# Kernel tuning notes

Hardware: AMD Instinct MI355X
Metric: run time of the kernel (lower is better)

Reference implementation:

```python
import jax, jax.numpy as jnp
import numpy as np

N_HEADS = 16


def setup_inputs() -> dict:
    key = jax.random.key(0)
    ks = jax.random.split(key, 12)
    B, S, D = 2, 2048, 1024
    inp = {
        "query": jax.random.normal(ks[0], (B, S, D), jnp.float32),
        "key": jax.random.normal(ks[1], (B, S, D), jnp.float32),
        "value": jax.random.normal(ks[2], (B, S, D), jnp.float32),
        "mask": jnp.ones((B, S), jnp.int32),
        "Wq": jax.random.normal(ks[3], (D, D), jnp.float32) * 0.02,
        "bq": jax.random.normal(ks[4], (D,), jnp.float32) * 0.02,
        "Wk": jax.random.normal(ks[5], (D, D), jnp.float32) * 0.02,
        "bk": jax.random.normal(ks[6], (D,), jnp.float32) * 0.02,
        "Wv": jax.random.normal(ks[7], (D, D), jnp.float32) * 0.02,
        "bv": jax.random.normal(ks[8], (D,), jnp.float32) * 0.02,
        "Wo": jax.random.normal(ks[9], (D, D), jnp.float32) * 0.02,
        "bo": jax.random.normal(ks[10], (D,), jnp.float32) * 0.02,
    }
    return inp


def _shape(x, bs, n_heads, d_head):
    # (bs, seq, dim) -> (bs, n_heads, seq, d_head)
    return x.reshape(bs, -1, n_heads, d_head).transpose(0, 2, 1, 3)


def reference(query, key, value, mask, Wq, bq, Wk, bk, Wv, bv, Wo, bo):
    bs, q_len, dim = query.shape
    d_head = dim // N_HEADS

    q = _shape(query @ Wq + bq, bs, N_HEADS, d_head) / jnp.sqrt(jnp.asarray(d_head, query.dtype))
    k = _shape(key @ Wk + bk, bs, N_HEADS, d_head)
    v = _shape(value @ Wv + bv, bs, N_HEADS, d_head)

    scores = jnp.einsum("bhqd,bhkd->bhqk", q, k)  # [bs, h, q_len, k_len]
    neg = jnp.finfo(scores.dtype).min
    scores = jnp.where((mask == 0)[:, None, None, :], neg, scores)
    weights = jax.nn.softmax(scores, axis=-1)  # dropout p=0 -> identity

    context = jnp.einsum("bhqk,bhkd->bhqd", weights, v)
    context = context.transpose(0, 2, 1, 3).reshape(bs, q_len, dim)
    return context @ Wo + bo
```

## Files before the change

### kernel.cpp

```cpp
#include <hip/hip_runtime.h>
#include <hip/hip_bf16.h>
#include <stdint.h>

typedef short s16x8 __attribute__((ext_vector_type(8)));
typedef float f32x4 __attribute__((ext_vector_type(4)));
typedef float f32x16 __attribute__((ext_vector_type(16)));

union FragU { uint4 u; s16x8 v; };

static __device__ __forceinline__ uint32_t pk2bf(float a, float b) {
  union { __hip_bfloat162 h; uint32_t u; } cv;
  cv.h = __float22bfloat162_rn(make_float2(a, b));
  return cv.u;
}

static __device__ __forceinline__ unsigned short f2bf(float f) {
  union { float f; uint32_t u; } x; x.f = f;
  uint32_t r = x.u + 0x7FFFu + ((x.u >> 16) & 1u);
  return (unsigned short)(r >> 16);
}

static __device__ __forceinline__ void gl_lds16(const void* g, void* lds_wave_base) {
  __builtin_amdgcn_global_load_lds(
      (const __attribute__((address_space(1))) uint32_t*)(uintptr_t)g,
      (__attribute__((address_space(3))) uint32_t*)(uintptr_t)lds_wave_base, 16, 0, 0);
}

__global__ __launch_bounds__(256) void wt4_kernel(const float* __restrict__ W0,
                                                  const float* __restrict__ W1,
                                                  const float* __restrict__ W2,
                                                  const float* __restrict__ W3,
                                                  unsigned short* __restrict__ T0,
                                                  unsigned short* __restrict__ T1,
                                                  unsigned short* __restrict__ T2,
                                                  unsigned short* __restrict__ T3) {
  __shared__ unsigned short tile[64][68];
  const int z = blockIdx.z;
  const float* W = (z == 0) ? W0 : (z == 1) ? W1 : (z == 2) ? W2 : W3;
  unsigned short* WT = (z == 0) ? T0 : (z == 1) ? T1 : (z == 2) ? T2 : T3;
  const int t = threadIdx.x;
  const int n0 = blockIdx.x * 64, k0 = blockIdx.y * 64;
  const int r = t >> 4, c4 = (t & 15) * 4;
#pragma unroll
  for (int i = 0; i < 4; ++i) {
    const int k = i * 16 + r;
    const float4 v = *(const float4*)&W[(k0 + k) * 1024 + n0 + c4];
    tile[k][c4 + 0] = f2bf(v.x);
    tile[k][c4 + 1] = f2bf(v.y);
    tile[k][c4 + 2] = f2bf(v.z);
    tile[k][c4 + 3] = f2bf(v.w);
  }
  __syncthreads();
#pragma unroll
  for (int i = 0; i < 4; ++i) {
    const int n = i * 16 + r;
    ushort4 o;
    o.x = tile[c4 + 0][n];
    o.y = tile[c4 + 1][n];
    o.z = tile[c4 + 2][n];
    o.w = tile[c4 + 3][n];
    *(ushort4*)&WT[(n0 + n) * 1024 + k0 + c4] = o;
  }
}

__global__ __launch_bounds__(256, 2) void qkv_gemm(const float* __restrict__ Aq,
                                                   const float* __restrict__ Ak,
                                                   const float* __restrict__ Av,
                                                   const unsigned short* __restrict__ Wq,
                                                   const unsigned short* __restrict__ Wk,
                                                   const unsigned short* __restrict__ Wv,
                                                   const float* __restrict__ bq,
                                                   const float* __restrict__ bk,
                                                   const float* __restrict__ bv,
                                                   unsigned short* __restrict__ Qb,
                                                   unsigned short* __restrict__ Kb,
                                                   unsigned short* __restrict__ Vt,
                                                   const float qscale) {
  __shared__ char AsB[3][128 * 128];
  __shared__ char BsB[3][128 * 64];
  const int t = threadIdx.x;
  const int z = blockIdx.z;
  const float* A = (z == 0) ? Aq : (z == 1) ? Ak : Av;
  const unsigned short* BT = (z == 0) ? Wq : (z == 1) ? Wk : Wv;
  const float* bias = (z == 0) ? bq : (z == 1) ? bk : bv;
  const float scale = (z == 0) ? qscale : 1.0f;

  const int lane = t & 63, w = t >> 6;
  const int g = lane >> 4, li = lane & 15;
  const int wr = (w >> 1) * 64, wc = (w & 1) * 64;
  const int lin = blockIdx.x + 8 * blockIdx.y;
  const int work = (lin & 7) * 32 + (lin >> 3);
  const int m0 = (work >> 3) * 128, n0 = (work & 7) * 128;

  const int br1 = t >> 2, bg1 = (t & 3) ^ ((br1 >> 1) & 3);
  const int br2 = br1 + 64, bg2 = (t & 3) ^ ((br2 >> 1) & 3);
  int arow[4], acol[4];
#pragma unroll
  for (int i = 0; i < 4; ++i) {
    const int c = t + 256 * i;
    const int row = c >> 3, sl = (c >> 1) & 3, hf = c & 1;
    arow[i] = row;
    acol[i] = ((sl ^ (row & 3)) << 3) + ((hf ^ ((row >> 2) & 1)) << 2);
  }

  auto stage = [&](int kt, int buf) {
    const int k0 = kt * 32;
    char* bb = &BsB[buf][0] + (w << 10);
    gl_lds16(BT + (size_t)(n0 + br1) * 1024 + k0 + bg1 * 8, bb);
    gl_lds16(BT + (size_t)(n0 + br2) * 1024 + k0 + bg2 * 8, bb + 4096);
#pragma unroll
    for (int i = 0; i < 4; ++i)
      gl_lds16(A + (size_t)(m0 + arow[i]) * 1024 + k0 + acol[i],
               &AsB[buf][0] + i * 4096 + (w << 10));
  };

  f32x4 acc[4][4] = {};
  stage(0, 0);
  stage(1, 1);
  asm volatile("s_waitcnt vmcnt(6)" ::: "memory");
  asm volatile("s_barrier" ::: "memory");

  int cur = 0;
  for (int kt = 0; kt < 32; ++kt) {
    if (kt < 30) {
      int nb = cur + 2; if (nb >= 3) nb -= 3;
      stage(kt + 2, nb);
    }
    const char* Ab = &AsB[cur][0];
    const char* Bb = &BsB[cur][0];
    FragU a[4], bf[4];
#pragma unroll
    for (int i = 0; i < 4; ++i) {
      const int ra = wr + i * 16 + li;
      const int hsw = ((ra >> 2) & 1) << 4;
      const char* pa = Ab + ra * 128 + ((g ^ (ra & 3)) << 5);
      const float4 fa0 = *(const float4*)(pa + hsw);
      const float4 fa1 = *(const float4*)(pa + (16 ^ hsw));
      a[i].u = uint4{pk2bf(fa0.x, fa0.y), pk2bf(fa0.z, fa0.w),
                     pk2bf(fa1.x, fa1.y), pk2bf(fa1.z, fa1.w)};
      const int rb = wc + i * 16 + li;
      bf[i].u = *(const uint4*)(Bb + rb * 64 + ((g ^ ((rb >> 1) & 3)) << 4));
    }
#pragma unroll
    for (int fm = 0; fm < 4; ++fm)
#pragma unroll
      for (int fn = 0; fn < 4; ++fn)
        acc[fm][fn] = __builtin_amdgcn_mfma_f32_16x16x32_bf16(a[fm].v, bf[fn].v, acc[fm][fn], 0, 0, 0);

    if (kt < 30) {
      asm volatile("s_waitcnt vmcnt(6)" ::: "memory");
    } else if (kt == 30) {
      asm volatile("s_waitcnt vmcnt(0)" ::: "memory");
    }
    if (kt < 31) asm volatile("s_barrier" ::: "memory");
    cur = (cur == 2) ? 0 : cur + 1;
  }

  unsigned short* OutN = (z == 0) ? Qb : Kb;
#pragma unroll
  for (int fn = 0; fn < 4; ++fn) {
    const int n = n0 + wc + fn * 16 + li;
    const float bv2 = bias[n];
#pragma unroll
    for (int fm = 0; fm < 4; ++fm) {
      const int mb = m0 + wr + fm * 16 + g * 4;
      const f32x4 v = acc[fm][fn];
      ushort4 pk;
      pk.x = f2bf((v[0] + bv2) * scale);
      pk.y = f2bf((v[1] + bv2) * scale);
      pk.z = f2bf((v[2] + bv2) * scale);
      pk.w = f2bf((v[3] + bv2) * scale);
      if (z == 2) {
        const int bb = mb >> 11, s = mb & 2047;
        *(ushort4*)&Vt[(size_t)(bb * 1024 + n) * 2048 + s] = pk;
      } else {
        unsigned short* o = OutN;
        o[(size_t)(mb + 0) * 1024 + n] = pk.x;
        o[(size_t)(mb + 1) * 1024 + n] = pk.y;
        o[(size_t)(mb + 2) * 1024 + n] = pk.z;
        o[(size_t)(mb + 3) * 1024 + n] = pk.w;
      }
    }
  }
}

__global__ __launch_bounds__(256, 2) void out_gemm(const unsigned short* __restrict__ A,
                                                   const unsigned short* __restrict__ BT,
                                                   const float* __restrict__ bias,
                                                   float* __restrict__ Out) {
  __shared__ char AsB[3][128 * 64];
  __shared__ char BsB[3][128 * 64];
  const int t = threadIdx.x;
  const int lane = t & 63, w = t >> 6;
  const int g = lane >> 4, li = lane & 15;
  const int wr = (w >> 1) * 64, wc = (w & 1) * 64;
  const int lin = blockIdx.x + 8 * blockIdx.y;
  const int work = (lin & 7) * 32 + (lin >> 3);
  const int m0 = (work >> 3) * 128, n0 = (work & 7) * 128;

  const int r1 = t >> 2, g1 = (t & 3) ^ ((r1 >> 1) & 3);
  const int r2 = r1 + 64, g2 = (t & 3) ^ ((r2 >> 1) & 3);

  auto stage = [&](int kt, int buf) {
    const int k0 = kt * 32;
    gl_lds16(BT + (size_t)(n0 + r1) * 1024 + k0 + g1 * 8, &BsB[buf][0] + (w << 10));
    gl_lds16(BT + (size_t)(n0 + r2) * 1024 + k0 + g2 * 8, &BsB[buf][0] + 4096 + (w << 10));
    gl_lds16(A + (size_t)(m0 + r1) * 1024 + k0 + g1 * 8, &AsB[buf][0] + (w << 10));
    gl_lds16(A + (size_t)(m0 + r2) * 1024 + k0 + g2 * 8, &AsB[buf][0] + 4096 + (w << 10));
  };

  f32x4 acc[4][4] = {};
  stage(0, 0);
  stage(1, 1);
  asm volatile("s_waitcnt vmcnt(4)" ::: "memory");
  asm volatile("s_barrier" ::: "memory");

  int cur = 0;
  for (int kt = 0; kt < 32; ++kt) {
    if (kt < 30) {
      int nb = cur + 2; if (nb >= 3) nb -= 3;
      stage(kt + 2, nb);
    }
    const char* Ab = &AsB[cur][0];
    const char* Bb = &BsB[cur][0];
    FragU a[4], bf[4];
#pragma unroll
    for (int i = 0; i < 4; ++i) {
      const int ra = wr + i * 16 + li;
      a[i].u = *(const uint4*)(Ab + ra * 64 + ((g ^ ((ra >> 1) & 3)) << 4));
      const int rb = wc + i * 16 + li;
      bf[i].u = *(const uint4*)(Bb + rb * 64 + ((g ^ ((rb >> 1) & 3)) << 4));
    }
#pragma unroll
    for (int fm = 0; fm < 4; ++fm)
#pragma unroll
      for (int fn = 0; fn < 4; ++fn)
        acc[fm][fn] = __builtin_amdgcn_mfma_f32_16x16x32_bf16(a[fm].v, bf[fn].v, acc[fm][fn], 0, 0, 0);

    if (kt < 30) {
      asm volatile("s_waitcnt vmcnt(4)" ::: "memory");
    } else if (kt == 30) {
      asm volatile("s_waitcnt vmcnt(0)" ::: "memory");
    }
    if (kt < 31) asm volatile("s_barrier" ::: "memory");
    cur = (cur == 2) ? 0 : cur + 1;
  }

#pragma unroll
  for (int fn = 0; fn < 4; ++fn) {
    const int n = n0 + wc + fn * 16 + li;
    const float bv = bias[n];
#pragma unroll
    for (int fm = 0; fm < 4; ++fm) {
      const int mb = m0 + wr + fm * 16 + g * 4;
      const f32x4 v = acc[fm][fn];
#pragma unroll
      for (int r = 0; r < 4; ++r) Out[(size_t)(mb + r) * 1024 + n] = v[r] + bv;
    }
  }
}

__global__ __launch_bounds__(256, 2) void attn_kernel(const unsigned short* __restrict__ Qb,
                                                      const unsigned short* __restrict__ Kb,
                                                      const unsigned short* __restrict__ Vt,
                                                      const int* __restrict__ mask,
                                                      unsigned short* __restrict__ ctx) {
  __shared__ unsigned short Ks[2][64 * 64];
  __shared__ unsigned short Vs[2][64 * 64];
  const int t = threadIdx.x, lane = t & 63, w = t >> 6;
  const int l31 = lane & 31, hi = lane >> 5;
  const int d0 = blockIdx.x + 16 * blockIdx.y;
  const int work = (d0 & 7) * 64 + (d0 >> 3);
  const int qblk = work & 15, bh = work >> 4;
  const int b = bh >> 4, h = bh & 15;
  const int q0 = qblk * 128;
  const int qrow = b * 2048 + q0 + w * 32 + l31;

  const int srow = t >> 3, sch = t & 7;

  uint4 kr0, kr1, vr0, vr1;
  int mv = 1;
  auto loadKV = [&](int kvn) {
    const unsigned short* kbase = Kb + (size_t)(b * 2048 + kvn) * 1024 + h * 64;
    kr0 = *(const uint4*)(kbase + (size_t)srow * 1024 + sch * 8);
    kr1 = *(const uint4*)(kbase + (size_t)(srow + 32) * 1024 + sch * 8);
    const unsigned short* vbase = Vt + (size_t)(b * 1024 + h * 64) * 2048 + kvn;
    vr0 = *(const uint4*)(vbase + (size_t)srow * 2048 + sch * 8);
    vr1 = *(const uint4*)(vbase + (size_t)(srow + 32) * 2048 + sch * 8);
    mv = mask[b * 2048 + kvn + lane];
  };
  auto storeKV = [&](int buf) {
    char* kb = (char*)&Ks[buf][0];
    char* vb = (char*)&Vs[buf][0];
    const int o0 = srow * 128 + ((sch * 16) ^ ((srow & 7) << 4));
    const int o1 = (srow + 32) * 128 + ((sch * 16) ^ ((srow & 7) << 4));
    *(uint4*)(kb + o0) = kr0;
    *(uint4*)(kb + o1) = kr1;
    *(uint4*)(vb + o0) = vr0;
    *(uint4*)(vb + o1) = vr1;
  };

  FragU qf[4];
  {
    const unsigned short* qb = Qb + (size_t)qrow * 1024 + h * 64 + hi * 8;
#pragma unroll
    for (int dc = 0; dc < 4; ++dc) qf[dc].u = *(const uint4*)(qb + dc * 16);
  }

  loadKV(0);
  storeKV(0);
  __syncthreads();

  f32x16 acc[2] = {};
  float m_run = 8.0f, l_run = 0.f;
  int cur = 0;

  for (int tile = 0; tile < 32; ++tile) {
    const bool more = tile + 1 < 32;
    const int mvcur = mv;
    if (more) loadKV((tile + 1) * 64);

    f32x16 sc[2] = {};
    {
      const char* kb = (const char*)&Ks[cur][0];
      __builtin_amdgcn_s_setprio(1);
#pragma unroll
      for (int t2 = 0; t2 < 2; ++t2) {
        const int row = t2 * 32 + l31;
        const int sw = (row & 7) << 4;
        const int rb = row * 128;
#pragma unroll
        for (int dc = 0; dc < 4; ++dc) {
          FragU kf;
          kf.u = *(const uint4*)(kb + rb + ((16 * (dc * 2 + hi)) ^ sw));
          sc[t2] = __builtin_amdgcn_mfma_f32_32x32x16_bf16(kf.v, qf[dc].v, sc[t2], 0, 0, 0);
        }
      }
      __builtin_amdgcn_s_setprio(0);
    }

    if (!__all(mvcur != 0)) {
#pragma unroll
      for (int t2 = 0; t2 < 2; ++t2)
#pragma unroll
        for (int r = 0; r < 16; ++r) {
          const int kvv = t2 * 32 + (r & 3) + 8 * (r >> 2) + 4 * hi;
          sc[t2][r] += (__shfl(mvcur, kvv, 64) ? 0.f : -30000.f);
        }
    }

    float pm = sc[0][0];
#pragma unroll
    for (int t2 = 0; t2 < 2; ++t2)
#pragma unroll
      for (int r = 0; r < 16; ++r) pm = fmaxf(pm, sc[t2][r]);
    pm = fmaxf(pm, __shfl_xor(pm, 32, 64));

    if (!__all(pm <= m_run + 8.f)) {
      const float m_new = fmaxf(m_run, pm);
      const float rsc = __builtin_amdgcn_exp2f(m_run - m_new);
      m_run = m_new;
      l_run *= rsc;
#pragma unroll
      for (int dt = 0; dt < 2; ++dt)
#pragma unroll
        for (int r = 0; r < 16; ++r) acc[dt][r] *= rsc;
    }

    float rs = 0.f;
#pragma unroll
    for (int t2 = 0; t2 < 2; ++t2)
#pragma unroll
      for (int r = 0; r < 16; ++r) {
        const float e = __builtin_amdgcn_exp2f(sc[t2][r] - m_run);
        sc[t2][r] = e;
        rs += e;
      }
    l_run += rs;

    FragU pf[4];
#pragma unroll
    for (int ks = 0; ks < 4; ++ks) {
      const int t2 = ks >> 1, s8 = (ks & 1) * 8;
      uint32_t U = pk2bf(sc[t2][s8 + 0], sc[t2][s8 + 1]);
      uint32_t V2 = pk2bf(sc[t2][s8 + 2], sc[t2][s8 + 3]);
      uint32_t X = pk2bf(sc[t2][s8 + 4], sc[t2][s8 + 5]);
      uint32_t Y = pk2bf(sc[t2][s8 + 6], sc[t2][s8 + 7]);
      asm("v_permlane32_swap_b32 %0, %1" : "+v"(U), "+v"(X));
      asm("v_permlane32_swap_b32 %0, %1" : "+v"(V2), "+v"(Y));
      pf[ks].u = uint4{U, V2, X, Y};
    }

    {
      const char* vb = (const char*)&Vs[cur][0];
      __builtin_amdgcn_s_setprio(1);
#pragma unroll
      for (int dt = 0; dt < 2; ++dt) {
        const int drow = dt * 32 + l31;
        const int sw = (drow & 7) << 4;
        const int rb = drow * 128;
#pragma unroll
        for (int ks = 0; ks < 4; ++ks) {
          FragU vf;
          vf.u = *(const uint4*)(vb + rb + ((16 * (ks * 2 + hi)) ^ sw));
          acc[dt] = __builtin_amdgcn_mfma_f32_32x32x16_bf16(vf.v, pf[ks].v, acc[dt], 0, 0, 0);
        }
      }
      __builtin_amdgcn_s_setprio(0);
    }

    if (more) storeKV(cur ^ 1);
    __syncthreads();
    cur ^= 1;
  }

  const float l_tot = l_run + __shfl_xor(l_run, 32, 64);
  const float inv_l = 1.0f / l_tot;
  unsigned short* cb = ctx + (size_t)qrow * 1024 + h * 64;
#pragma unroll
  for (int dt = 0; dt < 2; ++dt)
#pragma unroll
    for (int rq = 0; rq < 4; ++rq) {
      uint2 o;
      o.x = pk2bf(acc[dt][rq * 4 + 0] * inv_l, acc[dt][rq * 4 + 1] * inv_l);
      o.y = pk2bf(acc[dt][rq * 4 + 2] * inv_l, acc[dt][rq * 4 + 3] * inv_l);
      *(uint2*)(cb + dt * 32 + rq * 8 + hi * 4) = o;
    }
}

extern "C" void kernel_launch(void* const* d_in, const int* in_sizes, int n_in,
                              void* d_out, int out_size, void* d_ws, size_t ws_size,
                              hipStream_t stream) {
  const float* query = (const float*)d_in[0];
  const float* key = (const float*)d_in[1];
  const float* value = (const float*)d_in[2];
  const int* mask = (const int*)d_in[3];
  const float* Wq = (const float*)d_in[4];
  const float* bq = (const float*)d_in[5];
  const float* Wk = (const float*)d_in[6];
  const float* bk = (const float*)d_in[7];
  const float* Wv = (const float*)d_in[8];
  const float* bv = (const float*)d_in[9];
  const float* Wo = (const float*)d_in[10];
  const float* bo = (const float*)d_in[11];
  float* out = (float*)d_out;

  const size_t MB = 1024 * 1024;
  if (ws_size < 40 * MB) return;
  char* ws = (char*)d_ws;
  unsigned short* WqT = (unsigned short*)(ws);
  unsigned short* WkT = (unsigned short*)(ws + 2 * MB);
  unsigned short* WvT = (unsigned short*)(ws + 4 * MB);
  unsigned short* WoT = (unsigned short*)(ws + 6 * MB);
  unsigned short* Qb = (unsigned short*)(ws + 8 * MB);
  unsigned short* Kb = (unsigned short*)(ws + 16 * MB);
  unsigned short* Vt = (unsigned short*)(ws + 24 * MB);
  unsigned short* ctx = (unsigned short*)(ws + 32 * MB);

  const dim3 tb(256);
  wt4_kernel<<<dim3(16, 16, 4), tb, 0, stream>>>(Wq, Wk, Wv, Wo, WqT, WkT, WvT, WoT);

  const float qscale = 0.125f * 1.4426950408889634f;
  qkv_gemm<<<dim3(8, 32, 3), tb, 0, stream>>>(query, key, value, WqT, WkT, WvT,
                                              bq, bk, bv, Qb, Kb, Vt, qscale);

  attn_kernel<<<dim3(16, 32), tb, 0, stream>>>(Qb, Kb, Vt, mask, ctx);

  out_gemm<<<dim3(8, 32), tb, 0, stream>>>(ctx, WoT, bo, out);
}
```

Measured before the change: 139.2 us.

## Pre-convert QKV activations to bf16 before projection GEMM, with register-staged fallback

Adds a separate conversion kernel that turns the fp32 query/key/value tensors into bf16 in workspace, so the QKV GEMM can stage bf16 A tiles directly with async global-to-LDS loads and shrink LDS use. This removes the per-iteration fp32-to-bf16 packing and halves A-tile LDS footprint, letting occupancy rise to 3 blocks per CU. The cost is an extra kernel pass that reads and writes the activations, and it depends on a larger workspace. When the workspace is too small, a fallback uses register-staged fp32 loads with double buffering. The out GEMM is also set to 3 blocks per CU.

```diff
diff --git a/kernel.cpp b/kernel.cpp
--- a/kernel.cpp
+++ b/kernel.cpp
@@ -63,24 +63,40 @@
   }
 }
 
-__global__ __launch_bounds__(256, 2) void qkv_gemm(const float* __restrict__ Aq,
-                                                   const float* __restrict__ Ak,
-                                                   const float* __restrict__ Av,
-                                                   const unsigned short* __restrict__ Wq,
-                                                   const unsigned short* __restrict__ Wk,
-                                                   const unsigned short* __restrict__ Wv,
-                                                   const float* __restrict__ bq,
-                                                   const float* __restrict__ bk,
-                                                   const float* __restrict__ bv,
-                                                   unsigned short* __restrict__ Qb,
-                                                   unsigned short* __restrict__ Kb,
-                                                   unsigned short* __restrict__ Vt,
-                                                   const float qscale) {
-  __shared__ char AsB[3][128 * 128];
-  __shared__ char BsB[3][128 * 64];
+__global__ __launch_bounds__(256) void cvt3_kernel(const float* __restrict__ q,
+                                                   const float* __restrict__ k,
+                                                   const float* __restrict__ v,
+                                                   unsigned short* __restrict__ Qc,
+                                                   unsigned short* __restrict__ Kc,
+                                                   unsigned short* __restrict__ Vc) {
+  const int z = blockIdx.x >> 11, blk = blockIdx.x & 2047;
+  const float* src = (z == 0) ? q : (z == 1) ? k : v;
+  unsigned short* dst = (z == 0) ? Qc : (z == 1) ? Kc : Vc;
+  const size_t base = ((size_t)blk * 256 + threadIdx.x) * 8;
+  const float4 f0 = *(const float4*)(src + base);
+  const float4 f1 = *(const float4*)(src + base + 4);
+  const uint4 o{pk2bf(f0.x, f0.y), pk2bf(f0.z, f0.w), pk2bf(f1.x, f1.y), pk2bf(f1.z, f1.w)};
+  *(uint4*)(dst + base) = o;
+}
+
+__global__ __launch_bounds__(256, 3) void qkv_gemm_bf16(const unsigned short* __restrict__ Aq,
+                                                        const unsigned short* __restrict__ Ak,
+                                                        const unsigned short* __restrict__ Av,
+                                                        const unsigned short* __restrict__ Wq,
+                                                        const unsigned short* __restrict__ Wk,
+                                                        const unsigned short* __restrict__ Wv,
+                                                        const float* __restrict__ bq,
+                                                        const float* __restrict__ bk,
+                                                        const float* __restrict__ bv,
+                                                        unsigned short* __restrict__ Qb,
+                                                        unsigned short* __restrict__ Kb,
+                                                        unsigned short* __restrict__ Vt,
+                                                        const float qscale) {
+  __shared__ char AsB[3][8192];
+  __shared__ char BsB[3][8192];
   const int t = threadIdx.x;
   const int z = blockIdx.z;
-  const float* A = (z == 0) ? Aq : (z == 1) ? Ak : Av;
+  const unsigned short* A = (z == 0) ? Aq : (z == 1) ? Ak : Av;
   const unsigned short* BT = (z == 0) ? Wq : (z == 1) ? Wk : Wv;
   const float* bias = (z == 0) ? bq : (z == 1) ? bk : bv;
   const float scale = (z == 0) ? qscale : 1.0f;
@@ -92,32 +108,21 @@
   const int work = (lin & 7) * 32 + (lin >> 3);
   const int m0 = (work >> 3) * 128, n0 = (work & 7) * 128;
 
-  const int br1 = t >> 2, bg1 = (t & 3) ^ ((br1 >> 1) & 3);
-  const int br2 = br1 + 64, bg2 = (t & 3) ^ ((br2 >> 1) & 3);
-  int arow[4], acol[4];
-#pragma unroll
-  for (int i = 0; i < 4; ++i) {
-    const int c = t + 256 * i;
-    const int row = c >> 3, sl = (c >> 1) & 3, hf = c & 1;
-    arow[i] = row;
-    acol[i] = ((sl ^ (row & 3)) << 3) + ((hf ^ ((row >> 2) & 1)) << 2);
-  }
+  const int r1 = t >> 2, c1 = (t & 3) ^ ((r1 >> 1) & 3);
+  const int r2 = r1 + 64, c2 = (t & 3) ^ ((r2 >> 1) & 3);
 
   auto stage = [&](int kt, int buf) {
     const int k0 = kt * 32;
-    char* bb = &BsB[buf][0] + (w << 10);
-    gl_lds16(BT + (size_t)(n0 + br1) * 1024 + k0 + bg1 * 8, bb);
-    gl_lds16(BT + (size_t)(n0 + br2) * 1024 + k0 + bg2 * 8, bb + 4096);
-#pragma unroll
-    for (int i = 0; i < 4; ++i)
-      gl_lds16(A + (size_t)(m0 + arow[i]) * 1024 + k0 + acol[i],
-               &AsB[buf][0] + i * 4096 + (w << 10));
+    gl_lds16(A + (size_t)(m0 + r1) * 1024 + k0 + c1 * 8, &AsB[buf][0] + (w << 10));
+    gl_lds16(A + (size_t)(m0 + r2) * 1024 + k0 + c2 * 8, &AsB[buf][0] + 4096 + (w << 10));
+    gl_lds16(BT + (size_t)(n0 + r1) * 1024 + k0 + c1 * 8, &BsB[buf][0] + (w << 10));
+    gl_lds16(BT + (size_t)(n0 + r2) * 1024 + k0 + c2 * 8, &BsB[buf][0] + 4096 + (w << 10));
   };
 
   f32x4 acc[4][4] = {};
   stage(0, 0);
   stage(1, 1);
-  asm volatile("s_waitcnt vmcnt(6)" ::: "memory");
+  asm volatile("s_waitcnt vmcnt(4)" ::: "memory");
   asm volatile("s_barrier" ::: "memory");
 
   int cur = 0;
@@ -132,12 +137,7 @@
 #pragma unroll
     for (int i = 0; i < 4; ++i) {
       const int ra = wr + i * 16 + li;
-      const int hsw = ((ra >> 2) & 1) << 4;
-      const char* pa = Ab + ra * 128 + ((g ^ (ra & 3)) << 5);
-      const float4 fa0 = *(const float4*)(pa + hsw);
-      const float4 fa1 = *(const float4*)(pa + (16 ^ hsw));
-      a[i].u = uint4{pk2bf(fa0.x, fa0.y), pk2bf(fa0.z, fa0.w),
-                     pk2bf(fa1.x, fa1.y), pk2bf(fa1.z, fa1.w)};
+      a[i].u = *(const uint4*)(Ab + ra * 64 + ((g ^ ((ra >> 1) & 3)) << 4));
       const int rb = wc + i * 16 + li;
       bf[i].u = *(const uint4*)(Bb + rb * 64 + ((g ^ ((rb >> 1) & 3)) << 4));
     }
@@ -148,7 +148,7 @@
         acc[fm][fn] = __builtin_amdgcn_mfma_f32_16x16x32_bf16(a[fm].v, bf[fn].v, acc[fm][fn], 0, 0, 0);
 
     if (kt < 30) {
-      asm volatile("s_waitcnt vmcnt(6)" ::: "memory");
+      asm volatile("s_waitcnt vmcnt(4)" ::: "memory");
     } else if (kt == 30) {
       asm volatile("s_waitcnt vmcnt(0)" ::: "memory");
     }
@@ -184,12 +184,124 @@
   }
 }
 
-__global__ __launch_bounds__(256, 2) void out_gemm(const unsigned short* __restrict__ A,
+__global__ __launch_bounds__(256, 3) void qkv_gemm_f32(const float* __restrict__ Aq,
+                                                       const float* __restrict__ Ak,
+                                                       const float* __restrict__ Av,
+                                                       const unsigned short* __restrict__ Wq,
+                                                       const unsigned short* __restrict__ Wk,
+                                                       const unsigned short* __restrict__ Wv,
+                                                       const float* __restrict__ bq,
+                                                       const float* __restrict__ bk,
+                                                       const float* __restrict__ bv,
+                                                       unsigned short* __restrict__ Qb,
+                                                       unsigned short* __restrict__ Kb,
+                                                       unsigned short* __restrict__ Vt,
+                                                       const float qscale) {
+  __shared__ unsigned short As[2][128 * 32];
+  __shared__ unsigned short Bs[2][128 * 32];
+  const int t = threadIdx.x;
+  const int z = blockIdx.z;
+  const float* A = (z == 0) ? Aq : (z == 1) ? Ak : Av;
+  const unsigned short* BT = (z == 0) ? Wq : (z == 1) ? Wk : Wv;
+  const float* bias = (z == 0) ? bq : (z == 1) ? bk : bv;
+  const float scale = (z == 0) ? qscale : 1.0f;
+
+  const int lane = t & 63, w = t >> 6;
+  const int g = lane >> 4, li = lane & 15;
+  const int wr = (w >> 1) * 64, wc = (w & 1) * 64;
+  const int lin = blockIdx.x + 8 * blockIdx.y;
+  const int work = (lin & 7) * 32 + (lin >> 3);
+  const int m0 = (work >> 3) * 128, n0 = (work & 7) * 128;
+
+  const int arow = t >> 1, ac0 = (t & 1) * 2, asw = (arow >> 1) & 3;
+  const int br1 = t >> 2, bg1 = (t & 3) ^ ((br1 >> 1) & 3);
+  const int br2 = br1 + 64, bg2 = (t & 3) ^ ((br2 >> 1) & 3);
+
+  auto stageB = [&](int k0, int buf) {
+    gl_lds16(BT + (size_t)(n0 + br1) * 1024 + k0 + bg1 * 8, (char*)&Bs[buf][0] + (w << 10));
+    gl_lds16(BT + (size_t)(n0 + br2) * 1024 + k0 + bg2 * 8, (char*)&Bs[buf][0] + 4096 + (w << 10));
+  };
+
+  uint4 ar0, ar1;
+  auto loadA = [&](int k0) {
+    const float* ga = A + (size_t)(m0 + arow) * 1024 + k0 + ac0 * 8;
+    const float4 f0 = *(const float4*)(ga + 0), f1 = *(const float4*)(ga + 4);
+    const float4 f2 = *(const float4*)(ga + 8), f3 = *(const float4*)(ga + 12);
+    ar0 = uint4{pk2bf(f0.x, f0.y), pk2bf(f0.z, f0.w), pk2bf(f1.x, f1.y), pk2bf(f1.z, f1.w)};
+    ar1 = uint4{pk2bf(f2.x, f2.y), pk2bf(f2.z, f2.w), pk2bf(f3.x, f3.y), pk2bf(f3.z, f3.w)};
+  };
+  auto storeA = [&](int buf) {
+    char* ab = (char*)&As[buf][0] + arow * 64;
+    *(uint4*)(ab + ((ac0 ^ asw) << 4)) = ar0;
+    *(uint4*)(ab + (((ac0 + 1) ^ asw) << 4)) = ar1;
+  };
+
+  f32x4 acc[4][4] = {};
+  stageB(0, 0);
+  loadA(0);
+  storeA(0);
+  __syncthreads();
+  int cur = 0;
+  for (int k0 = 0; k0 < 1024; k0 += 32) {
+    const bool more = (k0 + 32) < 1024;
+    if (more) {
+      stageB(k0 + 32, cur ^ 1);
+      loadA(k0 + 32);
+    }
+    const char* Ab = (const char*)&As[cur][0];
+    const char* Bb = (const char*)&Bs[cur][0];
+    FragU a[4], bf[4];
+#pragma unroll
+    for (int i = 0; i < 4; ++i) {
+      const int rowa = wr + i * 16 + li;
+      a[i].u = *(const uint4*)(Ab + rowa * 64 + (((g) ^ ((rowa >> 1) & 3)) << 4));
+      const int rowb = wc + i * 16 + li;
+      bf[i].u = *(const uint4*)(Bb + rowb * 64 + (((g) ^ ((rowb >> 1) & 3)) << 4));
+    }
+#pragma unroll
+    for (int fm = 0; fm < 4; ++fm)
+#pragma unroll
+      for (int fn = 0; fn < 4; ++fn)
+        acc[fm][fn] = __builtin_amdgcn_mfma_f32_16x16x32_bf16(a[fm].v, bf[fn].v, acc[fm][fn], 0, 0, 0);
+    if (more) storeA(cur ^ 1);
+    __syncthreads();
+    cur ^= 1;
+  }
+
+  unsigned short* OutN = (z == 0) ? Qb : Kb;
+#pragma unroll
+  for (int fn = 0; fn < 4; ++fn) {
+    const int n = n0 + wc + fn * 16 + li;
+    const float bv2 = bias[n];
+#pragma unroll
+    for (int fm = 0; fm < 4; ++fm) {
+      const int mb = m0 + wr + fm * 16 + g * 4;
+      const f32x4 v = acc[fm][fn];
+      ushort4 pk;
+      pk.x = f2bf((v[0] + bv2) * scale);
+      pk.y = f2bf((v[1] + bv2) * scale);
+      pk.z = f2bf((v[2] + bv2) * scale);
+      pk.w = f2bf((v[3] + bv2) * scale);
+      if (z == 2) {
+        const int bb = mb >> 11, s = mb & 2047;
+        *(ushort4*)&Vt[(size_t)(bb * 1024 + n) * 2048 + s] = pk;
+      } else {
+        unsigned short* o = OutN;
+        o[(size_t)(mb + 0) * 1024 + n] = pk.x;
+        o[(size_t)(mb + 1) * 1024 + n] = pk.y;
+        o[(size_t)(mb + 2) * 1024 + n] = pk.z;
+        o[(size_t)(mb + 3) * 1024 + n] = pk.w;
+      }
+    }
+  }
+}
+
+__global__ __launch_bounds__(256, 3) void out_gemm(const unsigned short* __restrict__ A,
                                                    const unsigned short* __restrict__ BT,
                                                    const float* __restrict__ bias,
                                                    float* __restrict__ Out) {
-  __shared__ char AsB[3][128 * 64];
-  __shared__ char BsB[3][128 * 64];
+  __shared__ char AsB[3][8192];
+  __shared__ char BsB[3][8192];
   const int t = threadIdx.x;
   const int lane = t & 63, w = t >> 6;
   const int g = lane >> 4, li = lane & 15;
@@ -198,15 +310,15 @@
   const int work = (lin & 7) * 32 + (lin >> 3);
   const int m0 = (work >> 3) * 128, n0 = (work & 7) * 128;
 
-  const int r1 = t >> 2, g1 = (t & 3) ^ ((r1 >> 1) & 3);
-  const int r2 = r1 + 64, g2 = (t & 3) ^ ((r2 >> 1) & 3);
+  const int r1 = t >> 2, c1 = (t & 3) ^ ((r1 >> 1) & 3);
+  const int r2 = r1 + 64, c2 = (t & 3) ^ ((r2 >> 1) & 3);
 
   auto stage = [&](int kt, int buf) {
     const int k0 = kt * 32;
-    gl_lds16(BT + (size_t)(n0 + r1) * 1024 + k0 + g1 * 8, &BsB[buf][0] + (w << 10));
-    gl_lds16(BT + (size_t)(n0 + r2) * 1024 + k0 + g2 * 8, &BsB[buf][0] + 4096 + (w << 10));
-    gl_lds16(A + (size_t)(m0 + r1) * 1024 + k0 + g1 * 8, &AsB[buf][0] + (w << 10));
-    gl_lds16(A + (size_t)(m0 + r2) * 1024 + k0 + g2 * 8, &AsB[buf][0] + 4096 + (w << 10));
+    gl_lds16(A + (size_t)(m0 + r1) * 1024 + k0 + c1 * 8, &AsB[buf][0] + (w << 10));
+    gl_lds16(A + (size_t)(m0 + r2) * 1024 + k0 + c2 * 8, &AsB[buf][0] + 4096 + (w << 10));
+    gl_lds16(BT + (size_t)(n0 + r1) * 1024 + k0 + c1 * 8, &BsB[buf][0] + (w << 10));
+    gl_lds16(BT + (size_t)(n0 + r2) * 1024 + k0 + c2 * 8, &BsB[buf][0] + 4096 + (w << 10));
   };
 
   f32x4 acc[4][4] = {};
@@ -461,8 +573,18 @@
   wt4_kernel<<<dim3(16, 16, 4), tb, 0, stream>>>(Wq, Wk, Wv, Wo, WqT, WkT, WvT, WoT);
 
   const float qscale = 0.125f * 1.4426950408889634f;
-  qkv_gemm<<<dim3(8, 32, 3), tb, 0, stream>>>(query, key, value, WqT, WkT, WvT,
-                                              bq, bk, bv, Qb, Kb, Vt, qscale);
+
+  if (ws_size >= 64 * MB) {
+    unsigned short* Qc = (unsigned short*)(ws + 40 * MB);
+    unsigned short* Kc = (unsigned short*)(ws + 48 * MB);
+    unsigned short* Vc = (unsigned short*)(ws + 56 * MB);
+    cvt3_kernel<<<dim3(6144), tb, 0, stream>>>(query, key, value, Qc, Kc, Vc);
+    qkv_gemm_bf16<<<dim3(8, 32, 3), tb, 0, stream>>>(Qc, Kc, Vc, WqT, WkT, WvT,
+                                                     bq, bk, bv, Qb, Kb, Vt, qscale);
+  } else {
+    qkv_gemm_f32<<<dim3(8, 32, 3), tb, 0, stream>>>(query, key, value, WqT, WkT, WvT,
+                                                    bq, bk, bv, Qb, Kb, Vt, qscale);
+  }
 
   attn_kernel<<<dim3(16, 32), tb, 0, stream>>>(Qb, Kb, Vt, mask, ctx);
 
```

New measurement: 121.5 us. 12.7% less time.
